# Optimization experiments

Measured on AMD Instinct MI355X. Metric: run time of the kernel, lower is better.

Reference implementation:

```python
import jax, jax.numpy as jnp
import numpy as np

D_MODEL = 1024
NUM_HEADS = 16
HEAD_DIM = D_MODEL // NUM_HEADS


def setup_inputs() -> dict:
    key = jax.random.key(0)
    ks = jax.random.split(key, 6)
    B, S = 2, 2048
    w_scale = 1.0 / np.sqrt(D_MODEL)  # keep logits O(1) so the naive exp-softmax is stable
    return {
        "x": jax.random.normal(ks[0], (B, S, D_MODEL), dtype=jnp.float32),
        "y": jax.random.normal(ks[1], (B, S, D_MODEL), dtype=jnp.float32),
        "mask": jnp.zeros((S, S), dtype=jnp.float32),
        "Wq": jax.random.normal(ks[2], (D_MODEL, D_MODEL), dtype=jnp.float32) * w_scale,
        "Wk": jax.random.normal(ks[3], (D_MODEL, D_MODEL), dtype=jnp.float32) * w_scale,
        "Wv": jax.random.normal(ks[4], (D_MODEL, D_MODEL), dtype=jnp.float32) * w_scale,
        "Wo": jax.random.normal(ks[5], (D_MODEL, D_MODEL), dtype=jnp.float32) * w_scale,
    }


def _naive_softmax(s):
    # faithful to nirmalya_softmax: plain exp, sum + eps, no max subtraction
    p1 = jnp.exp(s)
    p2 = jnp.sum(p1, axis=-1, keepdims=True) + 1e-10
    return p1 / p2


def reference(x, y, mask, Wq, Wk, Wv, Wo):
    B, S, _ = x.shape
    # nn.Linear(bias=False): t @ W.T ; split heads -> [B, H, S, Dh]
    def split_heads(t):
        return t.reshape(B, S, NUM_HEADS, HEAD_DIM).transpose(0, 2, 1, 3)

    k = split_heads(x @ Wk.T)
    v = split_heads(x @ Wv.T)
    q = split_heads(y @ Wq.T)

    scores = jnp.einsum("bhqd,bhkd->bhqk", q, k) / np.sqrt(HEAD_DIM)
    scores = scores + mask  # [S,S] broadcasts over [B,H,S,S] (same math as permute-add-permute)
    attn = _naive_softmax(scores)
    out = jnp.einsum("bhqk,bhkd->bhqd", attn, v)  # [B,H,S,Dh]
    out = out.transpose(0, 2, 1, 3).reshape(B, S, D_MODEL)
    return out @ Wo.T
```

## Files before the change

kernel.cpp:

```cpp
#include <hip/hip_runtime.h>
#include <stdint.h>

typedef unsigned short u16;
typedef __attribute__((ext_vector_type(4))) float f32x4;
typedef __attribute__((ext_vector_type(2))) __bf16 bf16x2;
typedef __attribute__((ext_vector_type(8))) __bf16 bf16x8;
typedef __attribute__((ext_vector_type(4))) u16 u16x4;

#define AS1 __attribute__((address_space(1)))
#define AS3 __attribute__((address_space(3)))
#define GLOAD_LDS16(gp, lp) \
  __builtin_amdgcn_global_load_lds((const AS1 void*)(gp), (AS3 void*)(lp), 16, 0, 0)

__device__ __forceinline__ u16 f2bf(float f) {
  union { float f; unsigned u; } v; v.f = f;
  return (u16)((v.u + 0x7FFFu + ((v.u >> 16) & 1u)) >> 16);
}
__device__ __forceinline__ float bf2f(u16 u) {
  union { unsigned u; float f; } v; v.u = ((unsigned)u) << 16; return v.f;
}
__device__ __forceinline__ float fexp2(float x) {
#if __has_builtin(__builtin_amdgcn_exp2f)
  return __builtin_amdgcn_exp2f(x);
#else
  return exp2f(x);
#endif
}
__device__ __forceinline__ u16x4 pack4(float a, float b, float c, float d) {
#if __has_builtin(__builtin_amdgcn_cvt_pk_bf16_f32)
  union { struct { bf16x2 lo, hi; } p; u16x4 v; } u;
  u.p.lo = __builtin_amdgcn_cvt_pk_bf16_f32(a, b);
  u.p.hi = __builtin_amdgcn_cvt_pk_bf16_f32(c, d);
  return u.v;
#else
  u16x4 r; r.x = f2bf(a); r.y = f2bf(b); r.z = f2bf(c); r.w = f2bf(d); return r;
#endif
}

#define LOG2E 1.44269504f

__global__ __launch_bounds__(256) void convert_all(
    const float* __restrict__ x, const float* __restrict__ y,
    const float* __restrict__ wq, const float* __restrict__ wk,
    const float* __restrict__ wv, const float* __restrict__ wo,
    const float* __restrict__ mask,
    u16* __restrict__ xb, u16* __restrict__ yb, u16* __restrict__ wqb,
    u16* __restrict__ wkb, u16* __restrict__ wvb, u16* __restrict__ wob,
    u16* __restrict__ maskb) {
  size_t i = (size_t)blockIdx.x * 256 + threadIdx.x;
  const float* src; u16* dst; float scale = 1.0f; size_t off;
  if (i < (size_t)(1u << 20)) { src = x; dst = xb; off = i; }
  else if (i < (size_t)(2u << 20)) { src = y; dst = yb; off = i - (1u << 20); }
  else if (i < (size_t)(3u << 20)) {
    size_t j = i - (size_t)(2u << 20);
    unsigned w = (unsigned)(j >> 18); off = j & ((1u << 18) - 1);
    if (w == 0)      { src = wq; dst = wqb; scale = 0.125f * LOG2E; }
    else if (w == 1) { src = wk; dst = wkb; }
    else if (w == 2) { src = wv; dst = wvb; }
    else             { src = wo; dst = wob; }
  } else { src = mask; dst = maskb; scale = LOG2E; off = i - (size_t)(3u << 20); }
  f32x4 v = ((const f32x4*)src)[off];
  ((u16x4*)dst)[off] = pack4(v.x * scale, v.y * scale, v.z * scale, v.w * scale);
}

__device__ __forceinline__ void gemm_core64(
    const u16* __restrict__ A, const u16* __restrict__ Bt, int tm, int tn,
    u16* As, u16* Bs, f32x4 acc[4][4], int wave, int lane) {
  constexpr int K = 1024;
  const int l15 = lane & 15, quad = lane >> 4;
  const int wr = wave >> 1, wc = wave & 1;
  const int srow = lane >> 3;
  const int scol = ((lane & 7) ^ (srow & 7)) * 8;
  const u16* Ag = A + (size_t)(tm + wave * 32 + srow) * K + scol;
  const u16* Bg = Bt + (size_t)(tn + wave * 32 + srow) * K + scol;
  const int rsw = l15 & 7;

  for (int k0 = 0; k0 < K; k0 += 64) {
    __syncthreads();
#pragma unroll
    for (int c = 0; c < 4; ++c)
      GLOAD_LDS16(Ag + (size_t)c * 8 * K + k0, &As[(wave * 4 + c) * 512]);
#pragma unroll
    for (int c = 0; c < 4; ++c)
      GLOAD_LDS16(Bg + (size_t)c * 8 * K + k0, &Bs[(wave * 4 + c) * 512]);
    __syncthreads();
#pragma unroll
    for (int kq = 0; kq < 2; ++kq) {
      bf16x8 af[4], bfr[4];
#pragma unroll
      for (int mi = 0; mi < 4; ++mi)
        af[mi] = *(const bf16x8*)&As[(wr * 64 + mi * 16 + l15) * 64 +
                                     ((kq * 4 + quad) ^ rsw) * 8];
#pragma unroll
      for (int ni = 0; ni < 4; ++ni)
        bfr[ni] = *(const bf16x8*)&Bs[(wc * 64 + ni * 16 + l15) * 64 +
                                      ((kq * 4 + quad) ^ rsw) * 8];
#pragma unroll
      for (int mi = 0; mi < 4; ++mi)
#pragma unroll
        for (int ni = 0; ni < 4; ++ni)
          acc[mi][ni] = __builtin_amdgcn_mfma_f32_16x16x32_bf16(
              af[mi], bfr[ni], acc[mi][ni], 0, 0, 0);
    }
  }
}

__global__ __launch_bounds__(256, 3) void qkv_gemm(
    const u16* __restrict__ xb, const u16* __restrict__ yb,
    const u16* __restrict__ wqb, const u16* __restrict__ wkb,
    const u16* __restrict__ wvb,
    u16* __restrict__ Qw, u16* __restrict__ Kw, u16* __restrict__ Vtw) {
  __shared__ __align__(16) u16 As[128 * 64];
  __shared__ __align__(16) u16 Bs[128 * 64];
  const int tid = threadIdx.x, wave = tid >> 6, lane = tid & 63;
  const int l15 = lane & 15, quad = lane >> 4;
  const int wr = wave >> 1, wc = wave & 1;
  const int z = blockIdx.z;
  const u16 *A, *Bt; int tm, tn;
  if (z == 0)      { A = yb;  Bt = wqb; tm = blockIdx.y * 128; tn = blockIdx.x * 128; }
  else if (z == 1) { A = xb;  Bt = wkb; tm = blockIdx.y * 128; tn = blockIdx.x * 128; }
  else             { A = wvb; Bt = xb;  tm = blockIdx.x * 128; tn = blockIdx.y * 128; }

  f32x4 acc[4][4] = {};
  gemm_core64(A, Bt, tm, tn, As, Bs, acc, wave, lane);

#pragma unroll
  for (int mi = 0; mi < 4; ++mi) {
#pragma unroll
    for (int ni = 0; ni < 4; ++ni) {
#pragma unroll
      for (int r = 0; r < 4; ++r) {
        int gm = tm + wr * 64 + mi * 16 + quad * 4 + r;
        int gn = tn + wc * 64 + ni * 16 + l15;
        u16 val = f2bf(acc[mi][ni][r]);
        if (z == 2) {
          int h = gm >> 6, dh = gm & 63, b = gn >> 11, s = gn & 2047;
          Vtw[(((size_t)(b * 16 + h) * 64 + dh) << 11) + s] = val;
        } else {
          int b = gm >> 11, s = gm & 2047, h = gn >> 6, dh = gn & 63;
          u16* dst = (z == 0) ? Qw : Kw;
          dst[(((size_t)(b * 16 + h) * 2048 + s) << 6) + dh] = val;
        }
      }
    }
  }
}

__global__ __launch_bounds__(256, 3) void out_gemm(
    const u16* __restrict__ Ow, const u16* __restrict__ wob,
    float* __restrict__ C) {
  __shared__ __align__(16) u16 As[128 * 64];
  __shared__ __align__(16) u16 Bs[128 * 64];
  const int tid = threadIdx.x, wave = tid >> 6, lane = tid & 63;
  const int l15 = lane & 15, quad = lane >> 4;
  const int wr = wave >> 1, wc = wave & 1;
  const int tm = blockIdx.y * 128, tn = blockIdx.x * 128;

  f32x4 acc[4][4] = {};
  gemm_core64(Ow, wob, tm, tn, As, Bs, acc, wave, lane);

#pragma unroll
  for (int mi = 0; mi < 4; ++mi)
#pragma unroll
    for (int ni = 0; ni < 4; ++ni)
#pragma unroll
      for (int r = 0; r < 4; ++r) {
        int gm = tm + wr * 64 + mi * 16 + quad * 4 + r;
        int gn = tn + wc * 64 + ni * 16 + l15;
        C[(size_t)gm * 1024 + gn] = acc[mi][ni][r];
      }
}

__global__ __launch_bounds__(256, 2) void attn_kernel(
    const u16* __restrict__ Qw, const u16* __restrict__ Kw,
    const u16* __restrict__ Vtw, const u16* __restrict__ maskb,
    u16* __restrict__ Ow) {
  constexpr int S = 2048;
  constexpr int PADK = 136;
  __shared__ __align__(16) u16 Ks[128 * 64];
  __shared__ __align__(16) u16 Vs[64 * 128];
  __shared__ __align__(16) u16 Ps[128 * PADK];
  const int tid = threadIdx.x;
  const int wave = tid >> 6, lane = tid & 63;
  const int l15 = lane & 15, quad = lane >> 4;
  const int h = blockIdx.y, b = blockIdx.z;
  const size_t head = ((size_t)(b * 16 + h)) * S * 64;
  const int qbase = blockIdx.x * 128 + wave * 32;

  bf16x8 qf[2][2];
#pragma unroll
  for (int q2 = 0; q2 < 2; ++q2)
#pragma unroll
    for (int kq = 0; kq < 2; ++kq)
      qf[q2][kq] = *(const bf16x8*)&Qw[head +
          (size_t)(qbase + q2 * 16 + l15) * 64 + kq * 32 + quad * 8];

  const __bf16 one_bf = (__bf16)1.0f;
  const bf16x8 ones = {one_bf, one_bf, one_bf, one_bf, one_bf, one_bf, one_bf, one_bf};

  f32x4 oa[2][4] = {};
  f32x4 den[2] = {};

  const int k_key = lane >> 3;
  const int k_c = ((lane & 7) ^ (k_key & 7)) * 8;
  const int v_dh = lane >> 4;
  const int v_cl = lane & 15;
  const u16* mrow[2] = { maskb + (size_t)(qbase + l15) * S,
                         maskb + (size_t)(qbase + 16 + l15) * S };

  for (int kt = 0; kt < S; kt += 128) {
    __syncthreads();
#pragma unroll
    for (int c = 0; c < 4; ++c) {
      int g = wave * 4 + c;
      GLOAD_LDS16(&Kw[head + (size_t)(kt + g * 8 + k_key) * 64 + k_c], &Ks[g * 512]);
    }
#pragma unroll
    for (int c = 0; c < 4; ++c) {
      int g = wave * 4 + c;
      int dh = g * 4 + v_dh;
      GLOAD_LDS16(&Vtw[head + (size_t)dh * S + kt + ((v_cl ^ (dh & 15)) * 8)],
                  &Vs[g * 512]);
    }
    u16x4 mq[2][8];
#pragma unroll
    for (int q2 = 0; q2 < 2; ++q2)
#pragma unroll
      for (int mk = 0; mk < 8; ++mk)
        mq[q2][mk] = *(const u16x4*)&mrow[q2][kt + mk * 16 + quad * 4];
    __syncthreads();

    f32x4 sa[2][8] = {};
#pragma unroll
    for (int kq = 0; kq < 2; ++kq) {
#pragma unroll
      for (int mk = 0; mk < 8; ++mk) {
        bf16x8 ak = *(const bf16x8*)&Ks[(mk * 16 + l15) * 64 +
                                        ((kq * 4 + quad) ^ (l15 & 7)) * 8];
        sa[0][mk] = __builtin_amdgcn_mfma_f32_16x16x32_bf16(ak, qf[0][kq], sa[0][mk], 0, 0, 0);
        sa[1][mk] = __builtin_amdgcn_mfma_f32_16x16x32_bf16(ak, qf[1][kq], sa[1][mk], 0, 0, 0);
      }
    }

#pragma unroll
    for (int q2 = 0; q2 < 2; ++q2) {
#pragma unroll
      for (int mk = 0; mk < 8; ++mk) {
        float p0 = fexp2(sa[q2][mk][0] + bf2f(mq[q2][mk].x));
        float p1 = fexp2(sa[q2][mk][1] + bf2f(mq[q2][mk].y));
        float p2 = fexp2(sa[q2][mk][2] + bf2f(mq[q2][mk].z));
        float p3 = fexp2(sa[q2][mk][3] + bf2f(mq[q2][mk].w));
        *(u16x4*)&Ps[(wave * 32 + q2 * 16 + l15) * PADK + mk * 16 + quad * 4] =
            pack4(p0, p1, p2, p3);
      }
    }

#pragma unroll
    for (int kq2 = 0; kq2 < 4; ++kq2) {
      bf16x8 ap0 = *(const bf16x8*)&Ps[(wave * 32 + l15) * PADK + kq2 * 32 + quad * 8];
      bf16x8 ap1 = *(const bf16x8*)&Ps[(wave * 32 + 16 + l15) * PADK + kq2 * 32 + quad * 8];
#pragma unroll
      for (int nv = 0; nv < 4; ++nv) {
        bf16x8 bv = *(const bf16x8*)&Vs[(nv * 16 + l15) * 128 +
                                        ((kq2 * 4 + quad) ^ l15) * 8];
        oa[0][nv] = __builtin_amdgcn_mfma_f32_16x16x32_bf16(ap0, bv, oa[0][nv], 0, 0, 0);
        oa[1][nv] = __builtin_amdgcn_mfma_f32_16x16x32_bf16(ap1, bv, oa[1][nv], 0, 0, 0);
      }
      den[0] = __builtin_amdgcn_mfma_f32_16x16x32_bf16(ap0, ones, den[0], 0, 0, 0);
      den[1] = __builtin_amdgcn_mfma_f32_16x16x32_bf16(ap1, ones, den[1], 0, 0, 0);
    }
  }

#pragma unroll
  for (int q2 = 0; q2 < 2; ++q2) {
#pragma unroll
    for (int nv = 0; nv < 4; ++nv) {
#pragma unroll
      for (int r = 0; r < 4; ++r) {
        int srow = qbase + q2 * 16 + quad * 4 + r;
        int dh = nv * 16 + l15;
        float val = oa[q2][nv][r] / (den[q2][r] + 1e-10f);
        Ow[((size_t)(b * S + srow) << 10) + h * 64 + dh] = f2bf(val);
      }
    }
  }
}

extern "C" void kernel_launch(void* const* d_in, const int* in_sizes, int n_in,
                              void* d_out, int out_size, void* d_ws, size_t ws_size,
                              hipStream_t stream) {
  const float* x    = (const float*)d_in[0];
  const float* y    = (const float*)d_in[1];
  const float* mask = (const float*)d_in[2];
  const float* Wq   = (const float*)d_in[3];
  const float* Wk   = (const float*)d_in[4];
  const float* Wv   = (const float*)d_in[5];
  const float* Wo   = (const float*)d_in[6];
  char* ws = (char*)d_ws;
  const size_t MB = (size_t)1 << 20;
  u16* xb  = (u16*)(ws + 0  * MB);
  u16* yb  = (u16*)(ws + 8  * MB);
  u16* wqb = (u16*)(ws + 16 * MB);
  u16* wkb = (u16*)(ws + 18 * MB);
  u16* wvb = (u16*)(ws + 20 * MB);
  u16* wob = (u16*)(ws + 22 * MB);
  u16* Qw  = (u16*)(ws + 24 * MB);
  u16* Kw  = (u16*)(ws + 32 * MB);
  u16* Vtw = (u16*)(ws + 40 * MB);
  u16* Ow  = (u16*)(ws + 48 * MB);
  u16* maskb = (u16*)d_out;

  convert_all<<<16384, 256, 0, stream>>>(x, y, Wq, Wk, Wv, Wo, mask,
                                         xb, yb, wqb, wkb, wvb, wob, maskb);
  qkv_gemm<<<dim3(8, 32, 3), 256, 0, stream>>>(xb, yb, wqb, wkb, wvb, Qw, Kw, Vtw);
  attn_kernel<<<dim3(16, 16, 2), 256, 0, stream>>>(Qw, Kw, Vtw, maskb, Ow);
  out_gemm<<<dim3(8, 32), 256, 0, stream>>>(Ow, wob, (float*)d_out);
  (void)in_sizes; (void)n_in; (void)out_size; (void)ws_size;
}
```

Before: 246.3 us.

## Split attention over key halves with fp32 partials and a combine kernel

The attention kernel now splits the 2048 keys into two halves across grid z, so it launches twice as many blocks. Each block handles 64-key tiles with smaller LDS buffers and a higher occupancy bound, and writes unnormalized fp32 partial outputs and denominators. A new combine kernel sums the two partials, normalizes, and writes bf16 for the output GEMM. This targets under-occupancy, since 512 blocks is few for the GPU. In exchange it adds fp32 partial traffic, an extra launch, and more per-tile sync overhead. Workspace buffers are reused, and the mask is moved into workspace.

```diff
diff --git a/kernel.cpp b/kernel.cpp
--- a/kernel.cpp
+++ b/kernel.cpp
@@ -171,21 +171,23 @@
       }
 }
 
-__global__ __launch_bounds__(256, 2) void attn_kernel(
+__global__ __launch_bounds__(256, 4) void attn_kernel(
     const u16* __restrict__ Qw, const u16* __restrict__ Kw,
     const u16* __restrict__ Vtw, const u16* __restrict__ maskb,
-    u16* __restrict__ Ow) {
+    float* __restrict__ Op0, float* __restrict__ Op1, float* __restrict__ denb) {
   constexpr int S = 2048;
-  constexpr int PADK = 136;
-  __shared__ __align__(16) u16 Ks[128 * 64];
-  __shared__ __align__(16) u16 Vs[64 * 128];
+  constexpr int PADK = 72;
+  __shared__ __align__(16) u16 Ks[64 * 64];
+  __shared__ __align__(16) u16 Vs[64 * 64];
   __shared__ __align__(16) u16 Ps[128 * PADK];
   const int tid = threadIdx.x;
   const int wave = tid >> 6, lane = tid & 63;
   const int l15 = lane & 15, quad = lane >> 4;
-  const int h = blockIdx.y, b = blockIdx.z;
+  const int qt = blockIdx.x, h = blockIdx.y, z = blockIdx.z;
+  const int b = z >> 1, ks = z & 1;
   const size_t head = ((size_t)(b * 16 + h)) * S * 64;
-  const int qbase = blockIdx.x * 128 + wave * 32;
+  const int kbase = ks * 1024;
+  const int qbase = qt * 128 + wave * 32;
 
   bf16x8 qf[2][2];
 #pragma unroll
@@ -201,42 +203,40 @@
   f32x4 oa[2][4] = {};
   f32x4 den[2] = {};
 
-  const int k_key = lane >> 3;
-  const int k_c = ((lane & 7) ^ (k_key & 7)) * 8;
-  const int v_dh = lane >> 4;
-  const int v_cl = lane & 15;
-  const u16* mrow[2] = { maskb + (size_t)(qbase + l15) * S,
-                         maskb + (size_t)(qbase + 16 + l15) * S };
-
-  for (int kt = 0; kt < S; kt += 128) {
+  const int s_r = lane >> 3;
+  const int s_c = ((lane & 7) ^ s_r) * 8;
+  const int rsw = l15 & 7;
+
+  for (int kt = 0; kt < 1024; kt += 64) {
     __syncthreads();
 #pragma unroll
-    for (int c = 0; c < 4; ++c) {
-      int g = wave * 4 + c;
-      GLOAD_LDS16(&Kw[head + (size_t)(kt + g * 8 + k_key) * 64 + k_c], &Ks[g * 512]);
-    }
-#pragma unroll
-    for (int c = 0; c < 4; ++c) {
-      int g = wave * 4 + c;
-      int dh = g * 4 + v_dh;
-      GLOAD_LDS16(&Vtw[head + (size_t)dh * S + kt + ((v_cl ^ (dh & 15)) * 8)],
-                  &Vs[g * 512]);
-    }
-    u16x4 mq[2][8];
+    for (int c = 0; c < 2; ++c) {
+      int g = wave * 2 + c;
+      GLOAD_LDS16(&Kw[head + (size_t)(kbase + kt + g * 8 + s_r) * 64 + s_c],
+                  &Ks[g * 512]);
+    }
+#pragma unroll
+    for (int c = 0; c < 2; ++c) {
+      int g = wave * 2 + c;
+      int dh = g * 8 + s_r;
+      GLOAD_LDS16(&Vtw[head + (size_t)dh * S + kbase + kt + s_c], &Vs[g * 512]);
+    }
+    u16x4 mq[2][4];
 #pragma unroll
     for (int q2 = 0; q2 < 2; ++q2)
 #pragma unroll
-      for (int mk = 0; mk < 8; ++mk)
-        mq[q2][mk] = *(const u16x4*)&mrow[q2][kt + mk * 16 + quad * 4];
+      for (int mk = 0; mk < 4; ++mk)
+        mq[q2][mk] = *(const u16x4*)&maskb[(size_t)(qbase + q2 * 16 + l15) * S +
+                                           kbase + kt + mk * 16 + quad * 4];
     __syncthreads();
 
-    f32x4 sa[2][8] = {};
+    f32x4 sa[2][4] = {};
 #pragma unroll
     for (int kq = 0; kq < 2; ++kq) {
 #pragma unroll
-      for (int mk = 0; mk < 8; ++mk) {
+      for (int mk = 0; mk < 4; ++mk) {
         bf16x8 ak = *(const bf16x8*)&Ks[(mk * 16 + l15) * 64 +
-                                        ((kq * 4 + quad) ^ (l15 & 7)) * 8];
+                                        ((kq * 4 + quad) ^ rsw) * 8];
         sa[0][mk] = __builtin_amdgcn_mfma_f32_16x16x32_bf16(ak, qf[0][kq], sa[0][mk], 0, 0, 0);
         sa[1][mk] = __builtin_amdgcn_mfma_f32_16x16x32_bf16(ak, qf[1][kq], sa[1][mk], 0, 0, 0);
       }
@@ -245,7 +245,7 @@
 #pragma unroll
     for (int q2 = 0; q2 < 2; ++q2) {
 #pragma unroll
-      for (int mk = 0; mk < 8; ++mk) {
+      for (int mk = 0; mk < 4; ++mk) {
         float p0 = fexp2(sa[q2][mk][0] + bf2f(mq[q2][mk].x));
         float p1 = fexp2(sa[q2][mk][1] + bf2f(mq[q2][mk].y));
         float p2 = fexp2(sa[q2][mk][2] + bf2f(mq[q2][mk].z));
@@ -256,13 +256,13 @@
     }
 
 #pragma unroll
-    for (int kq2 = 0; kq2 < 4; ++kq2) {
+    for (int kq2 = 0; kq2 < 2; ++kq2) {
       bf16x8 ap0 = *(const bf16x8*)&Ps[(wave * 32 + l15) * PADK + kq2 * 32 + quad * 8];
       bf16x8 ap1 = *(const bf16x8*)&Ps[(wave * 32 + 16 + l15) * PADK + kq2 * 32 + quad * 8];
 #pragma unroll
       for (int nv = 0; nv < 4; ++nv) {
-        bf16x8 bv = *(const bf16x8*)&Vs[(nv * 16 + l15) * 128 +
-                                        ((kq2 * 4 + quad) ^ l15) * 8];
+        bf16x8 bv = *(const bf16x8*)&Vs[(nv * 16 + l15) * 64 +
+                                        ((kq2 * 4 + quad) ^ rsw) * 8];
         oa[0][nv] = __builtin_amdgcn_mfma_f32_16x16x32_bf16(ap0, bv, oa[0][nv], 0, 0, 0);
         oa[1][nv] = __builtin_amdgcn_mfma_f32_16x16x32_bf16(ap1, bv, oa[1][nv], 0, 0, 0);
       }
@@ -271,6 +271,7 @@
     }
   }
 
+  float* Op = ks ? Op1 : Op0;
 #pragma unroll
   for (int q2 = 0; q2 < 2; ++q2) {
 #pragma unroll
@@ -279,11 +280,36 @@
       for (int r = 0; r < 4; ++r) {
         int srow = qbase + q2 * 16 + quad * 4 + r;
         int dh = nv * 16 + l15;
-        float val = oa[q2][nv][r] / (den[q2][r] + 1e-10f);
-        Ow[((size_t)(b * S + srow) << 10) + h * 64 + dh] = f2bf(val);
-      }
-    }
-  }
+        Op[((size_t)(b * S + srow) << 10) + h * 64 + dh] = oa[q2][nv][r];
+      }
+    }
+  }
+  if (l15 == 0) {
+#pragma unroll
+    for (int q2 = 0; q2 < 2; ++q2)
+#pragma unroll
+      for (int r = 0; r < 4; ++r) {
+        int srow = qbase + q2 * 16 + quad * 4 + r;
+        denb[((size_t)(ks * 2 + b) * 16 + h) * 2048 + srow] = den[q2][r];
+      }
+  }
+}
+
+__global__ __launch_bounds__(256) void combine(
+    const float* __restrict__ Op0, const float* __restrict__ Op1,
+    const float* __restrict__ denb, u16* __restrict__ Ow) {
+  size_t i = (size_t)blockIdx.x * 256 + threadIdx.x;
+  size_t flat = i * 4;
+  int c = (int)(flat & 1023), h = c >> 6;
+  int s = (int)((flat >> 10) & 2047);
+  int b = (int)(flat >> 21);
+  f32x4 a = ((const f32x4*)Op0)[i];
+  f32x4 d = ((const f32x4*)Op1)[i];
+  float dn = denb[((size_t)b * 16 + h) * 2048 + s] +
+             denb[((size_t)(2 + b) * 16 + h) * 2048 + s] + 1e-10f;
+  float r = 1.0f / dn;
+  ((u16x4*)Ow)[i] = pack4((a.x + d.x) * r, (a.y + d.y) * r,
+                          (a.z + d.z) * r, (a.w + d.w) * r);
 }
 
 extern "C" void kernel_launch(void* const* d_in, const int* in_sizes, int n_in,
@@ -308,12 +334,16 @@
   u16* Kw  = (u16*)(ws + 32 * MB);
   u16* Vtw = (u16*)(ws + 40 * MB);
   u16* Ow  = (u16*)(ws + 48 * MB);
-  u16* maskb = (u16*)d_out;
+  u16* maskb = (u16*)(ws + 56 * MB);
+  float* Op0  = (float*)(ws + 0 * MB);
+  float* Op1  = (float*)d_out;
+  float* denb = (float*)(ws + 16 * MB);
 
   convert_all<<<16384, 256, 0, stream>>>(x, y, Wq, Wk, Wv, Wo, mask,
                                          xb, yb, wqb, wkb, wvb, wob, maskb);
   qkv_gemm<<<dim3(8, 32, 3), 256, 0, stream>>>(xb, yb, wqb, wkb, wvb, Qw, Kw, Vtw);
-  attn_kernel<<<dim3(16, 16, 2), 256, 0, stream>>>(Qw, Kw, Vtw, maskb, Ow);
+  attn_kernel<<<dim3(16, 16, 4), 256, 0, stream>>>(Qw, Kw, Vtw, maskb, Op0, Op1, denb);
+  combine<<<4096, 256, 0, stream>>>(Op0, Op1, denb, Ow);
   out_gemm<<<dim3(8, 32), 256, 0, stream>>>(Ow, wob, (float*)d_out);
   (void)in_sizes; (void)n_in; (void)out_size; (void)ws_size;
 }
```

New measurement: 295.9 us. 1.2x slower.

## Split attention keys across wave pairs with per-wave double-buffered K/V loads

Applied to the files above, without the earlier changes.

Restructures the attention kernel so that each pair of waves shares 64 query rows and splits the key range between them. Each wave streams its own 32-key K/V tiles into private double-buffered LDS with waitcnt instead of block-wide barriers, and prefetches mask values one step ahead. The two halves' partial outputs and denominators are combined through LDS at the end. The output GEMM also drops to 64-row tiles with an inline loop, doubling the grid, and the mask buffer moves into the workspace. The aim is to overlap loads with compute and cut barrier stalls, at the cost of a final cross-wave reduction and smaller per-iteration MFMA batches.

```diff
diff --git a/kernel.cpp b/kernel.cpp
--- a/kernel.cpp
+++ b/kernel.cpp
@@ -149,23 +149,56 @@
 __global__ __launch_bounds__(256, 3) void out_gemm(
     const u16* __restrict__ Ow, const u16* __restrict__ wob,
     float* __restrict__ C) {
-  __shared__ __align__(16) u16 As[128 * 64];
+  constexpr int K = 1024;
+  __shared__ __align__(16) u16 As[64 * 64];
   __shared__ __align__(16) u16 Bs[128 * 64];
   const int tid = threadIdx.x, wave = tid >> 6, lane = tid & 63;
   const int l15 = lane & 15, quad = lane >> 4;
   const int wr = wave >> 1, wc = wave & 1;
-  const int tm = blockIdx.y * 128, tn = blockIdx.x * 128;
-
-  f32x4 acc[4][4] = {};
-  gemm_core64(Ow, wob, tm, tn, As, Bs, acc, wave, lane);
-
-#pragma unroll
-  for (int mi = 0; mi < 4; ++mi)
+  const int tm = blockIdx.y * 64, tn = blockIdx.x * 128;
+  const int srow = lane >> 3;
+  const int scol = ((lane & 7) ^ (srow & 7)) * 8;
+  const u16* Ag = Ow + (size_t)(tm + wave * 16 + srow) * K + scol;
+  const u16* Bg = wob + (size_t)(tn + wave * 32 + srow) * K + scol;
+  const int rsw = l15 & 7;
+
+  f32x4 acc[2][4] = {};
+  for (int k0 = 0; k0 < K; k0 += 64) {
+    __syncthreads();
+#pragma unroll
+    for (int c = 0; c < 2; ++c)
+      GLOAD_LDS16(Ag + (size_t)c * 8 * K + k0, &As[(wave * 2 + c) * 512]);
+#pragma unroll
+    for (int c = 0; c < 4; ++c)
+      GLOAD_LDS16(Bg + (size_t)c * 8 * K + k0, &Bs[(wave * 4 + c) * 512]);
+    __syncthreads();
+#pragma unroll
+    for (int kq = 0; kq < 2; ++kq) {
+      bf16x8 af[2], bfr[4];
+#pragma unroll
+      for (int mi = 0; mi < 2; ++mi)
+        af[mi] = *(const bf16x8*)&As[(wr * 32 + mi * 16 + l15) * 64 +
+                                     ((kq * 4 + quad) ^ rsw) * 8];
+#pragma unroll
+      for (int ni = 0; ni < 4; ++ni)
+        bfr[ni] = *(const bf16x8*)&Bs[(wc * 64 + ni * 16 + l15) * 64 +
+                                      ((kq * 4 + quad) ^ rsw) * 8];
+#pragma unroll
+      for (int mi = 0; mi < 2; ++mi)
+#pragma unroll
+        for (int ni = 0; ni < 4; ++ni)
+          acc[mi][ni] = __builtin_amdgcn_mfma_f32_16x16x32_bf16(
+              af[mi], bfr[ni], acc[mi][ni], 0, 0, 0);
+    }
+  }
+
+#pragma unroll
+  for (int mi = 0; mi < 2; ++mi)
 #pragma unroll
     for (int ni = 0; ni < 4; ++ni)
 #pragma unroll
       for (int r = 0; r < 4; ++r) {
-        int gm = tm + wr * 64 + mi * 16 + quad * 4 + r;
+        int gm = tm + wr * 32 + mi * 16 + quad * 4 + r;
         int gn = tn + wc * 64 + ni * 16 + l15;
         C[(size_t)gm * 1024 + gn] = acc[mi][ni][r];
       }
@@ -176,111 +209,153 @@
     const u16* __restrict__ Vtw, const u16* __restrict__ maskb,
     u16* __restrict__ Ow) {
   constexpr int S = 2048;
-  constexpr int PADK = 136;
-  __shared__ __align__(16) u16 Ks[128 * 64];
-  __shared__ __align__(16) u16 Vs[64 * 128];
-  __shared__ __align__(16) u16 Ps[128 * PADK];
+  __shared__ __align__(16) u16 KV[4][2][4096];
+  __shared__ __align__(16) u16 Pbuf[4][2048];
   const int tid = threadIdx.x;
   const int wave = tid >> 6, lane = tid & 63;
   const int l15 = lane & 15, quad = lane >> 4;
   const int h = blockIdx.y, b = blockIdx.z;
   const size_t head = ((size_t)(b * 16 + h)) * S * 64;
-  const int qbase = blockIdx.x * 128 + wave * 32;
-
-  bf16x8 qf[2][2];
-#pragma unroll
-  for (int q2 = 0; q2 < 2; ++q2)
+  const int qbase = blockIdx.x * 128 + (wave >> 1) * 64;
+  const int kwb = (wave & 1) * 1024;
+
+  bf16x8 qf[4][2];
+#pragma unroll
+  for (int qt = 0; qt < 4; ++qt)
 #pragma unroll
     for (int kq = 0; kq < 2; ++kq)
-      qf[q2][kq] = *(const bf16x8*)&Qw[head +
-          (size_t)(qbase + q2 * 16 + l15) * 64 + kq * 32 + quad * 8];
+      qf[qt][kq] = *(const bf16x8*)&Qw[head +
+          (size_t)(qbase + qt * 16 + l15) * 64 + kq * 32 + quad * 8];
 
   const __bf16 one_bf = (__bf16)1.0f;
   const bf16x8 ones = {one_bf, one_bf, one_bf, one_bf, one_bf, one_bf, one_bf, one_bf};
 
-  f32x4 oa[2][4] = {};
-  f32x4 den[2] = {};
-
-  const int k_key = lane >> 3;
-  const int k_c = ((lane & 7) ^ (k_key & 7)) * 8;
-  const int v_dh = lane >> 4;
-  const int v_cl = lane & 15;
-  const u16* mrow[2] = { maskb + (size_t)(qbase + l15) * S,
-                         maskb + (size_t)(qbase + 16 + l15) * S };
-
-  for (int kt = 0; kt < S; kt += 128) {
-    __syncthreads();
-#pragma unroll
-    for (int c = 0; c < 4; ++c) {
-      int g = wave * 4 + c;
-      GLOAD_LDS16(&Kw[head + (size_t)(kt + g * 8 + k_key) * 64 + k_c], &Ks[g * 512]);
-    }
-#pragma unroll
-    for (int c = 0; c < 4; ++c) {
-      int g = wave * 4 + c;
-      int dh = g * 4 + v_dh;
-      GLOAD_LDS16(&Vtw[head + (size_t)dh * S + kt + ((v_cl ^ (dh & 15)) * 8)],
-                  &Vs[g * 512]);
-    }
-    u16x4 mq[2][8];
-#pragma unroll
-    for (int q2 = 0; q2 < 2; ++q2)
-#pragma unroll
-      for (int mk = 0; mk < 8; ++mk)
-        mq[q2][mk] = *(const u16x4*)&mrow[q2][kt + mk * 16 + quad * 4];
-    __syncthreads();
-
-    f32x4 sa[2][8] = {};
-#pragma unroll
-    for (int kq = 0; kq < 2; ++kq) {
-#pragma unroll
-      for (int mk = 0; mk < 8; ++mk) {
-        bf16x8 ak = *(const bf16x8*)&Ks[(mk * 16 + l15) * 64 +
-                                        ((kq * 4 + quad) ^ (l15 & 7)) * 8];
-        sa[0][mk] = __builtin_amdgcn_mfma_f32_16x16x32_bf16(ak, qf[0][kq], sa[0][mk], 0, 0, 0);
-        sa[1][mk] = __builtin_amdgcn_mfma_f32_16x16x32_bf16(ak, qf[1][kq], sa[1][mk], 0, 0, 0);
-      }
-    }
-
-#pragma unroll
-    for (int q2 = 0; q2 < 2; ++q2) {
-#pragma unroll
-      for (int mk = 0; mk < 8; ++mk) {
-        float p0 = fexp2(sa[q2][mk][0] + bf2f(mq[q2][mk].x));
-        float p1 = fexp2(sa[q2][mk][1] + bf2f(mq[q2][mk].y));
-        float p2 = fexp2(sa[q2][mk][2] + bf2f(mq[q2][mk].z));
-        float p3 = fexp2(sa[q2][mk][3] + bf2f(mq[q2][mk].w));
-        *(u16x4*)&Ps[(wave * 32 + q2 * 16 + l15) * PADK + mk * 16 + quad * 4] =
-            pack4(p0, p1, p2, p3);
-      }
-    }
-
-#pragma unroll
-    for (int kq2 = 0; kq2 < 4; ++kq2) {
-      bf16x8 ap0 = *(const bf16x8*)&Ps[(wave * 32 + l15) * PADK + kq2 * 32 + quad * 8];
-      bf16x8 ap1 = *(const bf16x8*)&Ps[(wave * 32 + 16 + l15) * PADK + kq2 * 32 + quad * 8];
+  f32x4 oa[4][4] = {};
+  f32x4 den[4] = {};
+  u16x4 mq[2][4][2];
+
+  const int k_r = lane >> 3;
+  const int k_c = ((lane & 7) ^ k_r) * 8;
+  const int v_r = lane >> 2;
+  const int v_c = (lane & 3) * 8;
+  const int rsw = l15 & 7;
+  u16* Ps = &Pbuf[wave][0];
+
+#pragma unroll
+  for (int c = 0; c < 4; ++c)
+    GLOAD_LDS16(&Kw[head + (size_t)(kwb + c * 8 + k_r) * 64 + k_c], &KV[wave][0][c * 512]);
+#pragma unroll
+  for (int c = 0; c < 4; ++c)
+    GLOAD_LDS16(&Vtw[head + (size_t)(c * 16 + v_r) * S + kwb + v_c], &KV[wave][0][2048 + c * 512]);
+#pragma unroll
+  for (int qt = 0; qt < 4; ++qt)
+#pragma unroll
+    for (int mk = 0; mk < 2; ++mk)
+      mq[0][qt][mk] = *(const u16x4*)&maskb[(size_t)(qbase + qt * 16 + l15) * S +
+                                            kwb + mk * 16 + quad * 4];
+
+#pragma unroll 1
+  for (int itb = 0; itb < 16; ++itb) {
+#pragma unroll
+    for (int half = 0; half < 2; ++half) {
+      const int it = itb * 2 + half;
+      __builtin_amdgcn_s_waitcnt(0);
+
+      if (it < 31) {
+        const int ko = kwb + (it + 1) * 32;
+#pragma unroll
+        for (int c = 0; c < 4; ++c)
+          GLOAD_LDS16(&Kw[head + (size_t)(ko + c * 8 + k_r) * 64 + k_c],
+                      &KV[wave][half ^ 1][c * 512]);
+#pragma unroll
+        for (int c = 0; c < 4; ++c)
+          GLOAD_LDS16(&Vtw[head + (size_t)(c * 16 + v_r) * S + ko + v_c],
+                      &KV[wave][half ^ 1][2048 + c * 512]);
+#pragma unroll
+        for (int qt = 0; qt < 4; ++qt)
+#pragma unroll
+          for (int mk = 0; mk < 2; ++mk)
+            mq[half ^ 1][qt][mk] = *(const u16x4*)&maskb[
+                (size_t)(qbase + qt * 16 + l15) * S + ko + mk * 16 + quad * 4];
+      }
+
+      const u16* Ks = &KV[wave][half][0];
+      const u16* Vs = &KV[wave][half][2048];
+
+      f32x4 sa[4][2] = {};
+#pragma unroll
+      for (int kq = 0; kq < 2; ++kq) {
+#pragma unroll
+        for (int mk = 0; mk < 2; ++mk) {
+          bf16x8 ak = *(const bf16x8*)&Ks[(mk * 16 + l15) * 64 +
+                                          ((kq * 4 + quad) ^ rsw) * 8];
+#pragma unroll
+          for (int qt = 0; qt < 4; ++qt)
+            sa[qt][mk] = __builtin_amdgcn_mfma_f32_16x16x32_bf16(
+                ak, qf[qt][kq], sa[qt][mk], 0, 0, 0);
+        }
+      }
+
+#pragma unroll
+      for (int qt = 0; qt < 4; ++qt) {
+#pragma unroll
+        for (int mk = 0; mk < 2; ++mk) {
+          float p0 = fexp2(sa[qt][mk][0] + bf2f(mq[half][qt][mk].x));
+          float p1 = fexp2(sa[qt][mk][1] + bf2f(mq[half][qt][mk].y));
+          float p2 = fexp2(sa[qt][mk][2] + bf2f(mq[half][qt][mk].z));
+          float p3 = fexp2(sa[qt][mk][3] + bf2f(mq[half][qt][mk].w));
+          *(u16x4*)&Ps[(qt * 16 + l15) * 32 + mk * 16 + quad * 4] =
+              pack4(p0, p1, p2, p3);
+        }
+      }
+
+#pragma unroll
+      for (int qt = 0; qt < 4; ++qt) {
+        bf16x8 ap = *(const bf16x8*)&Ps[(qt * 16 + l15) * 32 + quad * 8];
+#pragma unroll
+        for (int nv = 0; nv < 4; ++nv) {
+          bf16x8 bv = *(const bf16x8*)&Vs[(nv * 16 + l15) * 32 + quad * 8];
+          oa[qt][nv] = __builtin_amdgcn_mfma_f32_16x16x32_bf16(
+              ap, bv, oa[qt][nv], 0, 0, 0);
+        }
+        den[qt] = __builtin_amdgcn_mfma_f32_16x16x32_bf16(ap, ones, den[qt], 0, 0, 0);
+      }
+    }
+  }
+
+  __builtin_amdgcn_s_waitcnt(0);
+  if (!(wave & 1)) {
+    float* osc = (float*)&KV[wave][0][0];
+    float* dsc = (float*)&Pbuf[wave][0];
+#pragma unroll
+    for (int qt = 0; qt < 4; ++qt) {
+#pragma unroll
+      for (int nv = 0; nv < 4; ++nv)
+        *(f32x4*)&osc[(qt * 4 + nv) * 256 + lane * 4] = oa[qt][nv];
+      *(f32x4*)&dsc[qt * 256 + lane * 4] = den[qt];
+    }
+  }
+  __syncthreads();
+  if (wave & 1) {
+    const float* posc = (const float*)&KV[wave - 1][0][0];
+    const float* pdsc = (const float*)&Pbuf[wave - 1][0];
+#pragma unroll
+    for (int qt = 0; qt < 4; ++qt) {
+      f32x4 dsum = *(const f32x4*)&pdsc[qt * 256 + lane * 4];
+      f32x4 rd;
+#pragma unroll
+      for (int r = 0; r < 4; ++r)
+        rd[r] = __builtin_amdgcn_rcpf(dsum[r] + den[qt][r] + 1e-10f);
 #pragma unroll
       for (int nv = 0; nv < 4; ++nv) {
-        bf16x8 bv = *(const bf16x8*)&Vs[(nv * 16 + l15) * 128 +
-                                        ((kq2 * 4 + quad) ^ l15) * 8];
-        oa[0][nv] = __builtin_amdgcn_mfma_f32_16x16x32_bf16(ap0, bv, oa[0][nv], 0, 0, 0);
-        oa[1][nv] = __builtin_amdgcn_mfma_f32_16x16x32_bf16(ap1, bv, oa[1][nv], 0, 0, 0);
-      }
-      den[0] = __builtin_amdgcn_mfma_f32_16x16x32_bf16(ap0, ones, den[0], 0, 0, 0);
-      den[1] = __builtin_amdgcn_mfma_f32_16x16x32_bf16(ap1, ones, den[1], 0, 0, 0);
-    }
-  }
-
-#pragma unroll
-  for (int q2 = 0; q2 < 2; ++q2) {
-#pragma unroll
-    for (int nv = 0; nv < 4; ++nv) {
-#pragma unroll
-      for (int r = 0; r < 4; ++r) {
-        int srow = qbase + q2 * 16 + quad * 4 + r;
-        int dh = nv * 16 + l15;
-        float val = oa[q2][nv][r] / (den[q2][r] + 1e-10f);
-        Ow[((size_t)(b * S + srow) << 10) + h * 64 + dh] = f2bf(val);
+        f32x4 po = *(const f32x4*)&posc[(qt * 4 + nv) * 256 + lane * 4];
+#pragma unroll
+        for (int r = 0; r < 4; ++r) {
+          int q = qbase + qt * 16 + quad * 4 + r;
+          int dh = nv * 16 + l15;
+          Ow[((size_t)(b * S + q) << 10) + h * 64 + dh] =
+              f2bf((po[r] + oa[qt][nv][r]) * rd[r]);
+        }
       }
     }
   }
@@ -308,12 +383,12 @@
   u16* Kw  = (u16*)(ws + 32 * MB);
   u16* Vtw = (u16*)(ws + 40 * MB);
   u16* Ow  = (u16*)(ws + 48 * MB);
-  u16* maskb = (u16*)d_out;
+  u16* maskb = (u16*)(ws + 56 * MB);
 
   convert_all<<<16384, 256, 0, stream>>>(x, y, Wq, Wk, Wv, Wo, mask,
                                          xb, yb, wqb, wkb, wvb, wob, maskb);
   qkv_gemm<<<dim3(8, 32, 3), 256, 0, stream>>>(xb, yb, wqb, wkb, wvb, Qw, Kw, Vtw);
   attn_kernel<<<dim3(16, 16, 2), 256, 0, stream>>>(Qw, Kw, Vtw, maskb, Ow);
-  out_gemm<<<dim3(8, 32), 256, 0, stream>>>(Ow, wob, (float*)d_out);
+  out_gemm<<<dim3(8, 64), 256, 0, stream>>>(Ow, wob, (float*)d_out);
   (void)in_sizes; (void)n_in; (void)out_size; (void)ws_size;
 }
```

After: 238.9 us. -3.0%, faster.

## Keep softmax probabilities in registers via f16 MFMA, shrink out_gemm tile

Applied to the files above, without the earlier changes.

The attention kernel no longer writes P to a shared-memory buffer. Each 16-key chunk of exponentiated scores is packed into f16 registers and fed directly to a 16x16x16 f16 MFMA against V, which is now stored as fp16 by the QKV GEMM. Dropping the Ps buffer lowers LDS use so occupancy can go from 2 to 3 blocks per CU. The output GEMM moves to 64x128 tiles to launch more blocks, and the bf16 mask moves to its own workspace slot. The risks are fp16 range and precision limits on P and V, and the higher MFMA instruction count from the smaller K per instruction.

```diff
diff --git a/kernel.cpp b/kernel.cpp
--- a/kernel.cpp
+++ b/kernel.cpp
@@ -6,6 +6,8 @@
 typedef __attribute__((ext_vector_type(2))) __bf16 bf16x2;
 typedef __attribute__((ext_vector_type(8))) __bf16 bf16x8;
 typedef __attribute__((ext_vector_type(4))) u16 u16x4;
+typedef __attribute__((ext_vector_type(2))) _Float16 f16x2;
+typedef __attribute__((ext_vector_type(4))) _Float16 f16x4;
 
 #define AS1 __attribute__((address_space(1)))
 #define AS3 __attribute__((address_space(3)))
@@ -15,6 +17,9 @@
 __device__ __forceinline__ u16 f2bf(float f) {
   union { float f; unsigned u; } v; v.f = f;
   return (u16)((v.u + 0x7FFFu + ((v.u >> 16) & 1u)) >> 16);
+}
+__device__ __forceinline__ u16 f2h(float f) {
+  union { _Float16 h; u16 u; } v; v.h = (_Float16)f; return v.u;
 }
 __device__ __forceinline__ float bf2f(u16 u) {
   union { unsigned u; float f; } v; v.u = ((unsigned)u) << 16; return v.f;
@@ -24,6 +29,13 @@
   return __builtin_amdgcn_exp2f(x);
 #else
   return exp2f(x);
+#endif
+}
+__device__ __forceinline__ f16x2 pkf16(float a, float b) {
+#if __has_builtin(__builtin_amdgcn_cvt_pkrtz)
+  return __builtin_bit_cast(f16x2, __builtin_amdgcn_cvt_pkrtz(a, b));
+#else
+  f16x2 r; r.x = (_Float16)a; r.y = (_Float16)b; return r;
 #endif
 }
 __device__ __forceinline__ u16x4 pack4(float a, float b, float c, float d) {
@@ -132,14 +144,14 @@
       for (int r = 0; r < 4; ++r) {
         int gm = tm + wr * 64 + mi * 16 + quad * 4 + r;
         int gn = tn + wc * 64 + ni * 16 + l15;
-        u16 val = f2bf(acc[mi][ni][r]);
+        float val = acc[mi][ni][r];
         if (z == 2) {
           int h = gm >> 6, dh = gm & 63, b = gn >> 11, s = gn & 2047;
-          Vtw[(((size_t)(b * 16 + h) * 64 + dh) << 11) + s] = val;
+          Vtw[(((size_t)(b * 16 + h) * 64 + dh) << 11) + s] = f2h(val);
         } else {
           int b = gm >> 11, s = gm & 2047, h = gn >> 6, dh = gn & 63;
           u16* dst = (z == 0) ? Qw : Kw;
-          dst[(((size_t)(b * 16 + h) * 2048 + s) << 6) + dh] = val;
+          dst[(((size_t)(b * 16 + h) * 2048 + s) << 6) + dh] = f2bf(val);
         }
       }
     }
@@ -149,43 +161,74 @@
 __global__ __launch_bounds__(256, 3) void out_gemm(
     const u16* __restrict__ Ow, const u16* __restrict__ wob,
     float* __restrict__ C) {
-  __shared__ __align__(16) u16 As[128 * 64];
+  constexpr int K = 1024;
+  __shared__ __align__(16) u16 As[64 * 64];
   __shared__ __align__(16) u16 Bs[128 * 64];
   const int tid = threadIdx.x, wave = tid >> 6, lane = tid & 63;
   const int l15 = lane & 15, quad = lane >> 4;
   const int wr = wave >> 1, wc = wave & 1;
-  const int tm = blockIdx.y * 128, tn = blockIdx.x * 128;
-
-  f32x4 acc[4][4] = {};
-  gemm_core64(Ow, wob, tm, tn, As, Bs, acc, wave, lane);
-
-#pragma unroll
-  for (int mi = 0; mi < 4; ++mi)
+  const int tm = blockIdx.y * 64, tn = blockIdx.x * 128;
+  const int srow = lane >> 3;
+  const int scol = ((lane & 7) ^ (srow & 7)) * 8;
+  const u16* Ag = Ow + (size_t)(tm + wave * 16 + srow) * K + scol;
+  const u16* Bg = wob + (size_t)(tn + wave * 32 + srow) * K + scol;
+  const int rsw = l15 & 7;
+
+  f32x4 acc[2][4] = {};
+  for (int k0 = 0; k0 < K; k0 += 64) {
+    __syncthreads();
+#pragma unroll
+    for (int c = 0; c < 2; ++c)
+      GLOAD_LDS16(Ag + (size_t)c * 8 * K + k0, &As[(wave * 2 + c) * 512]);
+#pragma unroll
+    for (int c = 0; c < 4; ++c)
+      GLOAD_LDS16(Bg + (size_t)c * 8 * K + k0, &Bs[(wave * 4 + c) * 512]);
+    __syncthreads();
+#pragma unroll
+    for (int kq = 0; kq < 2; ++kq) {
+      bf16x8 af[2], bfr[4];
+#pragma unroll
+      for (int mi = 0; mi < 2; ++mi)
+        af[mi] = *(const bf16x8*)&As[(wr * 32 + mi * 16 + l15) * 64 +
+                                     ((kq * 4 + quad) ^ rsw) * 8];
+#pragma unroll
+      for (int ni = 0; ni < 4; ++ni)
+        bfr[ni] = *(const bf16x8*)&Bs[(wc * 64 + ni * 16 + l15) * 64 +
+                                      ((kq * 4 + quad) ^ rsw) * 8];
+#pragma unroll
+      for (int mi = 0; mi < 2; ++mi)
+#pragma unroll
+        for (int ni = 0; ni < 4; ++ni)
+          acc[mi][ni] = __builtin_amdgcn_mfma_f32_16x16x32_bf16(
+              af[mi], bfr[ni], acc[mi][ni], 0, 0, 0);
+    }
+  }
+
+#pragma unroll
+  for (int mi = 0; mi < 2; ++mi)
 #pragma unroll
     for (int ni = 0; ni < 4; ++ni)
 #pragma unroll
       for (int r = 0; r < 4; ++r) {
-        int gm = tm + wr * 64 + mi * 16 + quad * 4 + r;
+        int gm = tm + wr * 32 + mi * 16 + quad * 4 + r;
         int gn = tn + wc * 64 + ni * 16 + l15;
         C[(size_t)gm * 1024 + gn] = acc[mi][ni][r];
       }
 }
 
-__global__ __launch_bounds__(256, 2) void attn_kernel(
+__global__ __launch_bounds__(256, 3) void attn_kernel(
     const u16* __restrict__ Qw, const u16* __restrict__ Kw,
     const u16* __restrict__ Vtw, const u16* __restrict__ maskb,
     u16* __restrict__ Ow) {
   constexpr int S = 2048;
-  constexpr int PADK = 136;
   __shared__ __align__(16) u16 Ks[128 * 64];
   __shared__ __align__(16) u16 Vs[64 * 128];
-  __shared__ __align__(16) u16 Ps[128 * PADK];
   const int tid = threadIdx.x;
   const int wave = tid >> 6, lane = tid & 63;
   const int l15 = lane & 15, quad = lane >> 4;
-  const int h = blockIdx.y, b = blockIdx.z;
+  const int qt = blockIdx.x, h = blockIdx.y, b = blockIdx.z;
   const size_t head = ((size_t)(b * 16 + h)) * S * 64;
-  const int qbase = blockIdx.x * 128 + wave * 32;
+  const int qbase = qt * 128 + wave * 32;
 
   bf16x8 qf[2][2];
 #pragma unroll
@@ -195,30 +238,29 @@
       qf[q2][kq] = *(const bf16x8*)&Qw[head +
           (size_t)(qbase + q2 * 16 + l15) * 64 + kq * 32 + quad * 8];
 
-  const __bf16 one_bf = (__bf16)1.0f;
-  const bf16x8 ones = {one_bf, one_bf, one_bf, one_bf, one_bf, one_bf, one_bf, one_bf};
+  const _Float16 one_h = (_Float16)1.0f;
+  const f16x4 ones = {one_h, one_h, one_h, one_h};
 
   f32x4 oa[2][4] = {};
   f32x4 den[2] = {};
 
-  const int k_key = lane >> 3;
-  const int k_c = ((lane & 7) ^ (k_key & 7)) * 8;
-  const int v_dh = lane >> 4;
+  const int k_r = lane >> 3;
+  const int k_c = ((lane & 7) ^ k_r) * 8;
+  const int v_r = lane >> 4;
   const int v_cl = lane & 15;
-  const u16* mrow[2] = { maskb + (size_t)(qbase + l15) * S,
-                         maskb + (size_t)(qbase + 16 + l15) * S };
+  const int rsw = l15 & 7;
 
   for (int kt = 0; kt < S; kt += 128) {
     __syncthreads();
 #pragma unroll
     for (int c = 0; c < 4; ++c) {
       int g = wave * 4 + c;
-      GLOAD_LDS16(&Kw[head + (size_t)(kt + g * 8 + k_key) * 64 + k_c], &Ks[g * 512]);
+      GLOAD_LDS16(&Kw[head + (size_t)(kt + g * 8 + k_r) * 64 + k_c], &Ks[g * 512]);
     }
 #pragma unroll
     for (int c = 0; c < 4; ++c) {
       int g = wave * 4 + c;
-      int dh = g * 4 + v_dh;
+      int dh = g * 4 + v_r;
       GLOAD_LDS16(&Vtw[head + (size_t)dh * S + kt + ((v_cl ^ (dh & 15)) * 8)],
                   &Vs[g * 512]);
     }
@@ -227,47 +269,41 @@
     for (int q2 = 0; q2 < 2; ++q2)
 #pragma unroll
       for (int mk = 0; mk < 8; ++mk)
-        mq[q2][mk] = *(const u16x4*)&mrow[q2][kt + mk * 16 + quad * 4];
-    __syncthreads();
-
-    f32x4 sa[2][8] = {};
-#pragma unroll
-    for (int kq = 0; kq < 2; ++kq) {
-#pragma unroll
-      for (int mk = 0; mk < 8; ++mk) {
+        mq[q2][mk] = *(const u16x4*)&maskb[(size_t)(qbase + q2 * 16 + l15) * S +
+                                           kt + mk * 16 + quad * 4];
+    __syncthreads();
+
+#pragma unroll
+    for (int mk = 0; mk < 8; ++mk) {
+      f32x4 sa[2] = {};
+#pragma unroll
+      for (int kq = 0; kq < 2; ++kq) {
         bf16x8 ak = *(const bf16x8*)&Ks[(mk * 16 + l15) * 64 +
-                                        ((kq * 4 + quad) ^ (l15 & 7)) * 8];
-        sa[0][mk] = __builtin_amdgcn_mfma_f32_16x16x32_bf16(ak, qf[0][kq], sa[0][mk], 0, 0, 0);
-        sa[1][mk] = __builtin_amdgcn_mfma_f32_16x16x32_bf16(ak, qf[1][kq], sa[1][mk], 0, 0, 0);
-      }
-    }
-
-#pragma unroll
-    for (int q2 = 0; q2 < 2; ++q2) {
-#pragma unroll
-      for (int mk = 0; mk < 8; ++mk) {
-        float p0 = fexp2(sa[q2][mk][0] + bf2f(mq[q2][mk].x));
-        float p1 = fexp2(sa[q2][mk][1] + bf2f(mq[q2][mk].y));
-        float p2 = fexp2(sa[q2][mk][2] + bf2f(mq[q2][mk].z));
-        float p3 = fexp2(sa[q2][mk][3] + bf2f(mq[q2][mk].w));
-        *(u16x4*)&Ps[(wave * 32 + q2 * 16 + l15) * PADK + mk * 16 + quad * 4] =
-            pack4(p0, p1, p2, p3);
-      }
-    }
-
-#pragma unroll
-    for (int kq2 = 0; kq2 < 4; ++kq2) {
-      bf16x8 ap0 = *(const bf16x8*)&Ps[(wave * 32 + l15) * PADK + kq2 * 32 + quad * 8];
-      bf16x8 ap1 = *(const bf16x8*)&Ps[(wave * 32 + 16 + l15) * PADK + kq2 * 32 + quad * 8];
+                                        ((kq * 4 + quad) ^ rsw) * 8];
+        sa[0] = __builtin_amdgcn_mfma_f32_16x16x32_bf16(ak, qf[0][kq], sa[0], 0, 0, 0);
+        sa[1] = __builtin_amdgcn_mfma_f32_16x16x32_bf16(ak, qf[1][kq], sa[1], 0, 0, 0);
+      }
+      f16x4 pf[2];
+#pragma unroll
+      for (int q2 = 0; q2 < 2; ++q2) {
+        float p0 = fexp2(sa[q2][0] + bf2f(mq[q2][mk].x));
+        float p1 = fexp2(sa[q2][1] + bf2f(mq[q2][mk].y));
+        float p2 = fexp2(sa[q2][2] + bf2f(mq[q2][mk].z));
+        float p3 = fexp2(sa[q2][3] + bf2f(mq[q2][mk].w));
+        union { struct { f16x2 lo, hi; } p; f16x4 v; } u;
+        u.p.lo = pkf16(p0, p1); u.p.hi = pkf16(p2, p3);
+        pf[q2] = u.v;
+      }
 #pragma unroll
       for (int nv = 0; nv < 4; ++nv) {
-        bf16x8 bv = *(const bf16x8*)&Vs[(nv * 16 + l15) * 128 +
-                                        ((kq2 * 4 + quad) ^ l15) * 8];
-        oa[0][nv] = __builtin_amdgcn_mfma_f32_16x16x32_bf16(ap0, bv, oa[0][nv], 0, 0, 0);
-        oa[1][nv] = __builtin_amdgcn_mfma_f32_16x16x32_bf16(ap1, bv, oa[1][nv], 0, 0, 0);
-      }
-      den[0] = __builtin_amdgcn_mfma_f32_16x16x32_bf16(ap0, ones, den[0], 0, 0, 0);
-      den[1] = __builtin_amdgcn_mfma_f32_16x16x32_bf16(ap1, ones, den[1], 0, 0, 0);
+        f16x4 bv = *(const f16x4*)&Vs[(nv * 16 + l15) * 128 +
+                                      ((mk * 2 + (quad >> 1)) ^ l15) * 8 +
+                                      (quad & 1) * 4];
+        oa[0][nv] = __builtin_amdgcn_mfma_f32_16x16x16f16(pf[0], bv, oa[0][nv], 0, 0, 0);
+        oa[1][nv] = __builtin_amdgcn_mfma_f32_16x16x16f16(pf[1], bv, oa[1][nv], 0, 0, 0);
+      }
+      den[0] = __builtin_amdgcn_mfma_f32_16x16x16f16(pf[0], ones, den[0], 0, 0, 0);
+      den[1] = __builtin_amdgcn_mfma_f32_16x16x16f16(pf[1], ones, den[1], 0, 0, 0);
     }
   }
 
@@ -308,12 +344,12 @@
   u16* Kw  = (u16*)(ws + 32 * MB);
   u16* Vtw = (u16*)(ws + 40 * MB);
   u16* Ow  = (u16*)(ws + 48 * MB);
-  u16* maskb = (u16*)d_out;
+  u16* maskb = (u16*)(ws + 56 * MB);
 
   convert_all<<<16384, 256, 0, stream>>>(x, y, Wq, Wk, Wv, Wo, mask,
                                          xb, yb, wqb, wkb, wvb, wob, maskb);
   qkv_gemm<<<dim3(8, 32, 3), 256, 0, stream>>>(xb, yb, wqb, wkb, wvb, Qw, Kw, Vtw);
   attn_kernel<<<dim3(16, 16, 2), 256, 0, stream>>>(Qw, Kw, Vtw, maskb, Ow);
-  out_gemm<<<dim3(8, 32), 256, 0, stream>>>(Ow, wob, (float*)d_out);
+  out_gemm<<<dim3(8, 64), 256, 0, stream>>>(Ow, wob, (float*)d_out);
   (void)in_sizes; (void)n_in; (void)out_size; (void)ws_size;
 }
```

Result: faster. 233.7 us (-5.1%).
